# Optimization experiments

Measured on AMD Instinct MI355X. Metric: run time of the kernel, lower is better.

The kernel has to match this reference:

```python
import jax, jax.numpy as jnp
import numpy as np

EMBED = 1024
HEADS = 16
HEAD_SIZE = 64


def setup_inputs() -> dict:
    key = jax.random.key(0)
    ks = jax.random.split(key, 6)
    B, T = 2, 2048
    s = EMBED ** -0.5
    x = jax.random.normal(ks[0], (B, T, EMBED), dtype=jnp.float32)
    Wk = jax.random.normal(ks[1], (EMBED, HEADS * HEAD_SIZE), dtype=jnp.float32) * s
    Wq = jax.random.normal(ks[2], (EMBED, HEADS * HEAD_SIZE), dtype=jnp.float32) * s
    Wv = jax.random.normal(ks[3], (EMBED, HEADS * HEAD_SIZE), dtype=jnp.float32) * s
    Wp = jax.random.normal(ks[4], (HEADS * HEAD_SIZE, EMBED), dtype=jnp.float32) * s
    bp = jax.random.normal(ks[5], (EMBED,), dtype=jnp.float32) * 0.01
    return {"x": x, "Wk": Wk, "Wq": Wq, "Wv": Wv, "Wp": Wp, "bp": bp}


def reference(x, Wk, Wq, Wv, Wp, bp):
    # x: [B, T, C]; dropout in eval mode (identity), matching inference semantics
    B, T, C = x.shape
    def split_heads(y):  # [B,T,H*Dh] -> [B,H,T,Dh]
        return y.reshape(B, T, HEADS, HEAD_SIZE).transpose(0, 2, 1, 3)
    q = split_heads(x @ Wq)
    k = split_heads(x @ Wk)
    v = split_heads(x @ Wv)
    scale = HEAD_SIZE ** -0.5
    wei = jnp.einsum('bhqd,bhkd->bhqk', q, k) * scale  # [B,H,T,T]
    causal = jnp.tril(jnp.ones((T, T), dtype=bool))
    wei = jnp.where(causal, wei, -jnp.inf)
    wei = jax.nn.softmax(wei, axis=-1)
    out = jnp.einsum('bhqk,bhkd->bhqd', wei, v)  # [B,H,T,Dh]
    out = out.transpose(0, 2, 1, 3).reshape(B, T, HEADS * HEAD_SIZE)
    return out @ Wp + bp
```

## Files before the change

### kernel.cpp

```cpp
#include <hip/hip_runtime.h>
#include <stdint.h>


typedef unsigned short bfu;
typedef unsigned int u32;
typedef short bf16x8 __attribute__((ext_vector_type(8)));
typedef float f32x4 __attribute__((ext_vector_type(4)));
typedef float f32x16 __attribute__((ext_vector_type(16)));

#define DEVI static __device__ __forceinline__

DEVI bfu f2bf(float f) {
  union { float f; unsigned u; } a; a.f = f;
  unsigned u = a.u;
  u += 0x7fffu + ((u >> 16) & 1u);
  return (bfu)(u >> 16);
}

DEVI float bf2f(bfu x) {
  union { u32 u; float f; } a; a.u = ((u32)x) << 16; return a.f;
}

DEVI void gld_lds16(const void* g, void* l) {
  __builtin_amdgcn_global_load_lds(
      (const __attribute__((address_space(1))) void*)g,
      (__attribute__((address_space(3))) void*)l, 16, 0, 0);
}

#define BAR_VM4()                                         \
  do {                                                    \
    asm volatile("s_waitcnt vmcnt(4)" ::: "memory");      \
    __builtin_amdgcn_s_barrier();                         \
    asm volatile("" ::: "memory");                        \
  } while (0)
#define BAR_VM0()                                         \
  do {                                                    \
    asm volatile("s_waitcnt vmcnt(0)" ::: "memory");      \
    __builtin_amdgcn_s_barrier();                         \
    asm volatile("" ::: "memory");                        \
  } while (0)


__global__ __launch_bounds__(256) void conv_x(const float* __restrict__ x,
                                              bfu* __restrict__ xb) {
  const int n4 = (4096 * 1024) / 4;
  for (int i = blockIdx.x * 256 + threadIdx.x; i < n4; i += gridDim.x * 256) {
    float4 v = ((const float4*)x)[i];
    ushort4 p;
    p.x = f2bf(v.x); p.y = f2bf(v.y); p.z = f2bf(v.z); p.w = f2bf(v.w);
    ((ushort4*)xb)[i] = p;
  }
}

__global__ __launch_bounds__(256) void conv_w(
    const float* __restrict__ W0, const float* __restrict__ W1,
    const float* __restrict__ W2, const float* __restrict__ W3,
    bfu* __restrict__ T0, bfu* __restrict__ T1,
    bfu* __restrict__ T2, bfu* __restrict__ T3) {
  __shared__ bfu tile[64][65];
  const float* W; bfu* T;
  switch (blockIdx.z) {
    case 0:  W = W0; T = T0; break;
    case 1:  W = W1; T = T1; break;
    case 2:  W = W2; T = T2; break;
    default: W = W3; T = T3; break;
  }
  const int k0 = blockIdx.y * 64, n0 = blockIdx.x * 64;
  const int c = threadIdx.x & 63, r4 = threadIdx.x >> 6;
#pragma unroll
  for (int i = 0; i < 16; i++) {
    int row = r4 + i * 4;
    tile[row][c] = f2bf(W[(size_t)(k0 + row) * 1024 + n0 + c]);
  }
  __syncthreads();
#pragma unroll
  for (int i = 0; i < 16; i++) {
    int row = r4 + i * 4;
    T[(size_t)(n0 + row) * 1024 + k0 + c] = tile[c][row];
  }
}


__global__ __launch_bounds__(512) void gemm_qkv256(
    const bfu* __restrict__ A, const bfu* __restrict__ Bt,
    bfu* __restrict__ Qb, bfu* __restrict__ Kb, bfu* __restrict__ Vb) {
  __shared__ __align__(16) bfu LDS[2 * 32768];
  const int bid = blockIdx.x;
  const int xcd = bid & 7, i0 = bid >> 3;
  const int tx = i0 >> 1, ty = xcd * 2 + (i0 & 1);
  const int z = tx >> 2;
  const int m0 = ty * 256, n0g = tx * 256;
  const int tid = threadIdx.x, wave = tid >> 6, lane = tid & 63;
  const int wr = wave >> 2, wc = wave & 3;
  const int fr = lane & 15, fq = lane >> 4;
  const int rslot4 = fq ^ ((fr >> 1) & 3);

#define STAGE_HT(bufn, ktile, isB, kk)                                           \
  do {                                                                           \
    const bfu* srcb = (isB) ? Bt + (size_t)n0g * 1024 : A + (size_t)m0 * 1024;   \
    bfu* dstb = LDS + (bufn) * 32768 + ((isB) ? 16384 : 0) + (kk) * 8192;        \
    _Pragma("unroll")                                                            \
    for (int j_ = 0; j_ < 2; j_++) {                                             \
      int s_ = tid + j_ * 512;                                                   \
      int r_ = s_ >> 2, cg_ = (s_ & 3) ^ ((r_ >> 1) & 3);                        \
      gld_lds16(srcb + (size_t)r_ * 1024 + (ktile) * 64 + (kk) * 32 + cg_ * 8,   \
                dstb + s_ * 8);                                                  \
    }                                                                            \
  } while (0)

#define READ_B(kk)                                                               \
  _Pragma("unroll")                                                              \
  for (int n = 0; n < 4; n++)                                                    \
    bfv[n] = *(const bf16x8*)&bufc_p[16384 + (kk) * 8192 +                       \
              ((wc * 64 + n * 16 + fr) * 4 + rslot4) * 8];

#define READ_A(dst, mq, kk)                                                      \
  _Pragma("unroll")                                                              \
  for (int mm = 0; mm < 4; mm++)                                                 \
    dst[mm] = *(const bf16x8*)&bufc_p[(kk) * 8192 +                              \
              ((wr * 128 + ((mq) * 4 + mm) * 16 + fr) * 4 + rslot4) * 8];

#define MFMA_Q(afv, mq)                                                          \
  __builtin_amdgcn_s_setprio(1);                                                 \
  _Pragma("unroll")                                                              \
  for (int mm = 0; mm < 4; mm++)                                                 \
    _Pragma("unroll")                                                            \
    for (int n = 0; n < 4; n++)                                                  \
      acc[(mq) * 4 + mm][n] = __builtin_amdgcn_mfma_f32_16x16x32_bf16(           \
          afv[mm], bfv[n], acc[(mq) * 4 + mm][n], 0, 0, 0);                      \
  __builtin_amdgcn_s_setprio(0);

  f32x4 acc[8][4] = {};
  STAGE_HT(0, 0, 0, 0);
  STAGE_HT(0, 0, 1, 0);
  STAGE_HT(0, 0, 0, 1);
  STAGE_HT(0, 0, 1, 1);
  BAR_VM4();

  const int NT = 16;
  for (int t = 0; t < NT; t++) {
    const int more = (t + 1 < NT);
    const bfu* bufc_p = LDS + (t & 1) * 32768;
    const int bufn = (t & 1) ^ 1;
    bf16x8 bfv[4], afA[4], afB[4];
    READ_B(0);
    READ_A(afA, 0, 0);
    if (more) STAGE_HT(bufn, t + 1, 0, 0);
    MFMA_Q(afA, 0);
    READ_A(afB, 1, 0);
    if (more) STAGE_HT(bufn, t + 1, 1, 0);
    MFMA_Q(afB, 1);
    if (more) BAR_VM4();
    else      BAR_VM0();
    READ_B(1);
    READ_A(afA, 0, 1);
    if (more) STAGE_HT(bufn, t + 1, 0, 1);
    MFMA_Q(afA, 0);
    READ_A(afB, 1, 1);
    if (more) STAGE_HT(bufn, t + 1, 1, 1);
    MFMA_Q(afB, 1);
    BAR_VM4();
  }
#undef STAGE_HT
#undef READ_B
#undef READ_A
#undef MFMA_Q

  const float qs = (z == 0) ? 0.1803368801f : 1.0f;
#pragma unroll
  for (int mf = 0; mf < 8; mf++)
#pragma unroll
    for (int n = 0; n < 4; n++) {
      int r = m0 + wr * 128 + mf * 16 + fq * 4;
      int cwm = (tx & 3) * 256 + wc * 64 + n * 16 + fr;
      int b = r >> 11, tt = r & 2047, h = cwm >> 6, d = cwm & 63;
      if (z == 0) {
        size_t base = ((size_t)(b * 16 + h) * 2048 + tt) * 64 + d;
#pragma unroll
        for (int i = 0; i < 4; i++)
          Qb[base + (size_t)i * 64] = f2bf(acc[mf][n][i] * qs);
      } else if (z == 1) {
        size_t base = ((size_t)(b * 16 + h) * 2048 + tt) * 64 + d;
#pragma unroll
        for (int i = 0; i < 4; i++)
          Kb[base + (size_t)i * 64] = f2bf(acc[mf][n][i]);
      } else {
        size_t base = ((size_t)(b * 16 + h) * 64 + d) * 2048 + tt;
        ushort4 p;
        p.x = f2bf(acc[mf][n][0]); p.y = f2bf(acc[mf][n][1]);
        p.z = f2bf(acc[mf][n][2]); p.w = f2bf(acc[mf][n][3]);
        *(ushort4*)&Vb[base] = p;
      }
    }
}


DEVI void gemm128_core(const bfu* __restrict__ A, const bfu* __restrict__ Bt,
                       int K, int m0, int n0, bfu* As, bfu* Bs, int tid,
                       f32x4 acc[4][4]) {
  const int lane = tid & 63, wave = tid >> 6;
  const int wr = wave >> 1, wc = wave & 1;
  const int fr = lane & 15, fq = lane >> 4;
  const int r_a = tid >> 2;
  const int koff = ((tid & 3) ^ ((tid >> 3) & 3)) * 8;
  const int rslot = (fq ^ ((fr >> 1) & 3)) * 8;
#define GSTAGE(buf, k0s)                                                              \
  do {                                                                                \
    gld_lds16(A  + (size_t)(m0 +      r_a) * K + (k0s) + koff,                        \
              As + (buf) * 4096 + tid * 8);                                           \
    gld_lds16(A  + (size_t)(m0 + 64 + r_a) * K + (k0s) + koff,                        \
              As + (buf) * 4096 + 2048 + tid * 8);                                    \
    gld_lds16(Bt + (size_t)(n0 +      r_a) * K + (k0s) + koff,                        \
              Bs + (buf) * 4096 + tid * 8);                                           \
    gld_lds16(Bt + (size_t)(n0 + 64 + r_a) * K + (k0s) + koff,                        \
              Bs + (buf) * 4096 + 2048 + tid * 8);                                    \
  } while (0)
  const int NS = K >> 5;
  GSTAGE(0, 0);
  GSTAGE(1, 32);
  BAR_VM4();
  for (int i = 0; i < NS; i++) {
    if (i + 2 < NS) GSTAGE((i + 2) % 3, (i + 2) * 32);
    const bfu* AsC = As + (i % 3) * 4096;
    const bfu* BsC = Bs + (i % 3) * 4096;
    bf16x8 af[4], bfv[4];
#pragma unroll
    for (int m = 0; m < 4; m++)
      af[m] = *(const bf16x8*)&AsC[(wr * 64 + m * 16 + fr) * 32 + rslot];
#pragma unroll
    for (int n = 0; n < 4; n++)
      bfv[n] = *(const bf16x8*)&BsC[(wc * 64 + n * 16 + fr) * 32 + rslot];
#pragma unroll
    for (int m = 0; m < 4; m++)
#pragma unroll
      for (int n = 0; n < 4; n++)
        acc[m][n] = __builtin_amdgcn_mfma_f32_16x16x32_bf16(af[m], bfv[n],
                                                            acc[m][n], 0, 0, 0);
    if (i + 2 < NS) BAR_VM4();
    else            BAR_VM0();
  }
#undef GSTAGE
}

__global__ __launch_bounds__(256) void gemm_proj(
    const bfu* __restrict__ A, const bfu* __restrict__ Bt,
    const float* __restrict__ bias, float* __restrict__ out) {
  __shared__ __align__(16) bfu As[3 * 4096];
  __shared__ __align__(16) bfu Bs[3 * 4096];
  const int bid = blockIdx.x;
  const int xcd = bid & 7, i0 = bid >> 3;
  const int tx = i0 >> 2, ty = xcd * 4 + (i0 & 3);
  const int m0 = ty * 128, n0 = tx * 128;
  const int tid = threadIdx.x, lane = tid & 63, wave = tid >> 6;
  const int wr = wave >> 1, wc = wave & 1, fr = lane & 15, fq = lane >> 4;
  f32x4 acc[4][4] = {};
  gemm128_core(A, Bt, 1024, m0, n0, As, Bs, tid, acc);
#pragma unroll
  for (int m = 0; m < 4; m++)
#pragma unroll
    for (int n = 0; n < 4; n++) {
      int r = m0 + wr * 64 + m * 16 + fq * 4;
      int c = n0 + wc * 64 + n * 16 + fr;
      float bv = bias[c];
#pragma unroll
      for (int i = 0; i < 4; i++)
        out[(size_t)(r + i) * 1024 + c] = acc[m][n][i] + bv;
    }
}


__global__ __launch_bounds__(256) void attn_fwd(
    const bfu* __restrict__ Q, const bfu* __restrict__ K,
    const bfu* __restrict__ Vt, bfu* __restrict__ Ob,
    bfu* __restrict__ PO, float* __restrict__ PM, float* __restrict__ PL) {
  __shared__ __align__(16) bfu Ks[3][4096];
  __shared__ __align__(16) bfu Vs[3][4096];
  const int bid = blockIdx.x;
  const int xcd = bid & 7, i0 = bid >> 3;
  const int slot = i0 >> 5, cuL = i0 & 31;
  const int head = cuL >> 3, cu8 = cuL & 7;
  const int hb = xcd * 4 + head;
  int qb, mode;
  if (slot < 2)      { qb = 15 - cu8; mode = slot + 1; }
  else if (cu8 < 4)  { if (slot == 3) return; qb = cu8; mode = 0; }
  else               { qb = cu8; mode = slot - 1; }
  const int kb0   = (mode == 2) ? (qb + 1) : 0;
  const int kbmax = (mode == 1) ? qb : (2 * qb + 1);
  const int tid = threadIdx.x, wave = tid >> 6, lane = tid & 63;
  const int q31 = lane & 31, hi = lane >> 5;
  const bfu* Qh = Q  + (size_t)hb * 2048 * 64;
  const bfu* Kh = K  + (size_t)hb * 2048 * 64;
  const bfu* Vh = Vt + (size_t)hb * 64 * 2048;
  const int b = hb >> 4, h = hb & 15;
  const int q0w = qb * 128 + wave * 32;
  const int qg = q0w + q31;

  const int r0 = tid >> 3, r1 = (256 + tid) >> 3;
  const int c0 = (tid & 7) ^ (r0 & 7), c1 = (tid & 7) ^ (r1 & 7);
#define STAGE_K(bufi, kbase)                                                          \
  do {                                                                                \
    gld_lds16(Kh + (size_t)((kbase) + r0) * 64 + c0 * 8, &Ks[bufi][tid * 8]);         \
    gld_lds16(Kh + (size_t)((kbase) + r1) * 64 + c1 * 8, &Ks[bufi][(256 + tid) * 8]); \
  } while (0)
#define STAGE_V(bufi, kbase)                                                          \
  do {                                                                                \
    gld_lds16(Vh + (size_t)r0 * 2048 + (kbase) + c0 * 8, &Vs[bufi][tid * 8]);         \
    gld_lds16(Vh + (size_t)r1 * 2048 + (kbase) + c1 * 8, &Vs[bufi][(256 + tid) * 8]); \
  } while (0)

  bf16x8 qv[4];
#pragma unroll
  for (int c = 0; c < 4; c++)
    qv[c] = *(const bf16x8*)&Qh[(size_t)(q0w + q31) * 64 + c * 16 + hi * 8];

  bf16x8 onesv;
#pragma unroll
  for (int j = 0; j < 8; j++) onesv[j] = (short)0x3F80;

  f32x16 o0 = {}, o1 = {}, lac = {};
  float m = -1e30f;

  STAGE_K(0, kb0 * 64);
  STAGE_V(0, kb0 * 64);
  STAGE_K(1, (kb0 + 1) * 64);
  STAGE_V(1, (kb0 + 1) * 64);
  BAR_VM4();

  for (int kb = kb0; kb <= kbmax; kb++) {
    const int idx = kb - kb0;
    const int cur = idx % 3, nxt = (idx + 2) % 3;
    const int pre = (kb + 2 <= kbmax);
    const int kbase = kb * 64;
    const int active = (kbase <= q0w + 31);
    const bfu* KsC = Ks[cur];
    const bfu* VsC = Vs[cur];
    if (pre) STAGE_K(nxt, (kb + 2) * 64);
    u32 W0[8], W1[8];
    if (active) {
      f32x16 s0 = {}, s1 = {};
#pragma unroll
      for (int c = 0; c < 4; c++) {
        const int g = 2 * c + hi;
        bf16x8 kf0 = *(const bf16x8*)&KsC[(q31 * 8 + (g ^ (q31 & 7))) * 8];
        bf16x8 kf1 = *(const bf16x8*)&KsC[((32 + q31) * 8 + (g ^ (q31 & 7))) * 8];
        s0 = __builtin_amdgcn_mfma_f32_32x32x16_bf16(kf0, qv[c], s0, 0, 0, 0);
        s1 = __builtin_amdgcn_mfma_f32_32x32x16_bf16(kf1, qv[c], s1, 0, 0, 0);
      }
      if (kbase + 63 > q0w) {
#pragma unroll
        for (int r = 0; r < 16; r++) {
          int krow = (r & 3) + 8 * (r >> 2) + 4 * hi;
          if (kbase + krow > qg)      s0[r] = -1e30f;
          if (kbase + 32 + krow > qg) s1[r] = -1e30f;
        }
      }
      float pm = s0[0];
#pragma unroll
      for (int r = 1; r < 16; r++) pm = fmaxf(pm, s0[r]);
#pragma unroll
      for (int r = 0; r < 16; r++) pm = fmaxf(pm, s1[r]);
      pm = fmaxf(pm, __shfl_xor(pm, 32));
      if (!__all(pm <= m + 8.0f)) {
        float mn = fmaxf(m, pm);
        float al = __builtin_amdgcn_exp2f(m - mn);
        m = mn;
#pragma unroll
        for (int r = 0; r < 16; r++) {
          float alq = __shfl(al, (r & 3) + 8 * (r >> 2) + 4 * hi);
          o0[r] *= alq; o1[r] *= alq; lac[r] *= alq;
        }
      }
#pragma unroll
      for (int w = 0; w < 8; w++) {
        float a0 = __builtin_amdgcn_exp2f(s0[2 * w] - m);
        float a1 = __builtin_amdgcn_exp2f(s0[2 * w + 1] - m);
        asm("v_cvt_pk_bf16_f32 %0, %1, %2" : "=v"(W0[w]) : "v"(a0), "v"(a1));
        float b0 = __builtin_amdgcn_exp2f(s1[2 * w] - m);
        float b1 = __builtin_amdgcn_exp2f(s1[2 * w + 1] - m);
        asm("v_cvt_pk_bf16_f32 %0, %1, %2" : "=v"(W1[w]) : "v"(b0), "v"(b1));
      }
    }
    if (pre) STAGE_V(nxt, (kb + 2) * 64);
    if (active) {
      __builtin_amdgcn_s_setprio(1);
#pragma unroll
      for (int c = 0; c < 4; c++) {
        const u32* Wsel = (c < 2) ? W0 : W1;
        const int w0 = 4 * (c & 1);
        u32 t0 = Wsel[w0],     t2 = Wsel[w0 + 2];
        u32 t1 = Wsel[w0 + 1], t3 = Wsel[w0 + 3];
        asm("v_permlane32_swap_b32 %0, %1" : "+v"(t0), "+v"(t2));
        asm("v_permlane32_swap_b32 %0, %1" : "+v"(t1), "+v"(t3));
        union { u32 u[4]; bf16x8 v; } pa;
        pa.u[0] = t0; pa.u[1] = t1; pa.u[2] = t2; pa.u[3] = t3;
        const int g = 2 * c + hi;
        bf16x8 vb0 = *(const bf16x8*)&VsC[(q31 * 8 + (g ^ (q31 & 7))) * 8];
        bf16x8 vb1 = *(const bf16x8*)&VsC[((32 + q31) * 8 + (g ^ (q31 & 7))) * 8];
        o0  = __builtin_amdgcn_mfma_f32_32x32x16_bf16(pa.v, vb0,   o0,  0, 0, 0);
        o1  = __builtin_amdgcn_mfma_f32_32x32x16_bf16(pa.v, vb1,   o1,  0, 0, 0);
        lac = __builtin_amdgcn_mfma_f32_32x32x16_bf16(pa.v, onesv, lac, 0, 0, 0);
      }
      __builtin_amdgcn_s_setprio(0);
    }
    if (pre) BAR_VM4();
    else     BAR_VM0();
  }
#undef STAGE_K
#undef STAGE_V

  if (mode == 0) {
#pragma unroll
    for (int r = 0; r < 16; r++) {
      int t = q0w + (r & 3) + 8 * (r >> 2) + 4 * hi;
      float inv = 1.0f / lac[r];
      size_t base = (size_t)(b * 2048 + t) * 1024 + h * 64;
      Ob[base + q31]      = f2bf(o0[r] * inv);
      Ob[base + 32 + q31] = f2bf(o1[r] * inv);
    }
  } else {
    const int p = (hb * 12 + (qb - 4)) * 2 + (mode - 1);
    bfu*   po = PO + (size_t)p * 8192;
    float* pmv = PM + p * 128;
    float* plv = PL + p * 128;
    pmv[wave * 32 + q31] = m;
#pragma unroll
    for (int r = 0; r < 16; r++) {
      int rm = (r & 3) + 8 * (r >> 2) + 4 * hi;
      plv[wave * 32 + rm] = lac[r];
      po[(wave * 32 + rm) * 64 + q31]      = f2bf(o0[r]);
      po[(wave * 32 + rm) * 64 + 32 + q31] = f2bf(o1[r]);
    }
  }
}

__global__ __launch_bounds__(256) void attn_comb(
    const bfu* __restrict__ PO, const float* __restrict__ PM,
    const float* __restrict__ PL, bfu* __restrict__ Ob) {
  const int g = blockIdx.x;
  const int hb = g / 12, j = g % 12, qb = j + 4;
  const int b = hb >> 4, h = hb & 15;
  const int p0 = g * 2, p1 = p0 + 1;
  const int tid = threadIdx.x;
  const int r = tid >> 1, ch = tid & 1;
  float m0 = PM[p0 * 128 + r], m1 = PM[p1 * 128 + r];
  float l0 = PL[p0 * 128 + r], l1 = PL[p1 * 128 + r];
  float ms = fmaxf(m0, m1);
  float f0 = __builtin_amdgcn_exp2f(m0 - ms);
  float f1 = __builtin_amdgcn_exp2f(m1 - ms);
  float inv = 1.0f / (l0 * f0 + l1 * f1);
  const bfu* a0 = PO + (size_t)p0 * 8192 + r * 64 + ch * 32;
  const bfu* a1 = PO + (size_t)p1 * 8192 + r * 64 + ch * 32;
  const int t = qb * 128 + r;
  bfu* ob = Ob + (size_t)(b * 2048 + t) * 1024 + h * 64 + ch * 32;
#pragma unroll
  for (int k = 0; k < 4; k++) {
    bf16x8 v0 = *(const bf16x8*)(a0 + k * 8);
    bf16x8 v1 = *(const bf16x8*)(a1 + k * 8);
    bf16x8 vo;
#pragma unroll
    for (int e = 0; e < 8; e++) {
      float acc = bf2f((bfu)(unsigned short)v0[e]) * f0 +
                  bf2f((bfu)(unsigned short)v1[e]) * f1;
      vo[e] = (short)f2bf(acc * inv);
    }
    *(bf16x8*)(ob + k * 8) = vo;
  }
}


extern "C" void kernel_launch(void* const* d_in, const int* in_sizes, int n_in,
                              void* d_out, int out_size, void* d_ws, size_t ws_size,
                              hipStream_t stream) {
  const float* x  = (const float*)d_in[0];
  const float* Wk = (const float*)d_in[1];
  const float* Wq = (const float*)d_in[2];
  const float* Wv = (const float*)d_in[3];
  const float* Wp = (const float*)d_in[4];
  const float* bp = (const float*)d_in[5];
  char* ws = (char*)d_ws;
  bfu* xb  = (bfu*)(ws);
  bfu* Wqt = (bfu*)(ws + ( 8u << 20));
  bfu* Wkt = (bfu*)(ws + (10u << 20));
  bfu* Wvt = (bfu*)(ws + (12u << 20));
  bfu* Wpt = (bfu*)(ws + (14u << 20));
  bfu* Qb  = (bfu*)(ws + (16u << 20));
  bfu* Kb  = (bfu*)(ws + (24u << 20));
  bfu* Vb  = (bfu*)(ws + (32u << 20));
  bfu* Ab  = (bfu*)(ws + (40u << 20));
  bfu*   PO = (bfu*)(ws);
  float* PM = (float*)(ws + (13u << 20));
  float* PL = (float*)(ws + (13u << 20) + (512u << 10));
  float* out = (float*)d_out;

  conv_x<<<1024, 256, 0, stream>>>(x, xb);
  conv_w<<<dim3(16, 16, 4), 256, 0, stream>>>(Wq, Wk, Wv, Wp, Wqt, Wkt, Wvt, Wpt);
  gemm_qkv256<<<192, 512, 0, stream>>>(xb, Wqt, Qb, Kb, Vb);
  attn_fwd<<<1024, 256, 0, stream>>>(Qb, Kb, Vb, Ab, PO, PM, PL);
  attn_comb<<<384, 256, 0, stream>>>(PO, PM, PL, Ab);
  gemm_proj<<<256, 256, 0, stream>>>(Ab, Wpt, bp, out);
}
```

Baseline: 121.1 us.

## Rewrite projection GEMM with 512 threads, double-buffered K=64 tiles and split staging

The output projection GEMM goes from 256 to 512 threads per block, each of the 8 waves computing a 32x64 sub-tile. K advances in 64-wide tiles held in two LDS buffers. Each tile's loads are split into half-stages that are interleaved with MFMA groups, which run under raised s_setprio. The goal is more waves to hide latency and better overlap of loads with compute, at the cost of more barriers per K tile and fewer accumulators per wave.

```diff
diff --git a/kernel.cpp b/kernel.cpp
--- a/kernel.cpp
+++ b/kernel.cpp
@@ -30,6 +30,12 @@
 #define BAR_VM4()                                         \
   do {                                                    \
     asm volatile("s_waitcnt vmcnt(4)" ::: "memory");      \
+    __builtin_amdgcn_s_barrier();                         \
+    asm volatile("" ::: "memory");                        \
+  } while (0)
+#define BAR_VM2()                                         \
+  do {                                                    \
+    asm volatile("s_waitcnt vmcnt(2)" ::: "memory");      \
     __builtin_amdgcn_s_barrier();                         \
     asm volatile("" ::: "memory");                        \
   } while (0)
@@ -195,76 +201,94 @@
 }
 
 
-DEVI void gemm128_core(const bfu* __restrict__ A, const bfu* __restrict__ Bt,
-                       int K, int m0, int n0, bfu* As, bfu* Bs, int tid,
-                       f32x4 acc[4][4]) {
-  const int lane = tid & 63, wave = tid >> 6;
-  const int wr = wave >> 1, wc = wave & 1;
-  const int fr = lane & 15, fq = lane >> 4;
-  const int r_a = tid >> 2;
-  const int koff = ((tid & 3) ^ ((tid >> 3) & 3)) * 8;
-  const int rslot = (fq ^ ((fr >> 1) & 3)) * 8;
-#define GSTAGE(buf, k0s)                                                              \
-  do {                                                                                \
-    gld_lds16(A  + (size_t)(m0 +      r_a) * K + (k0s) + koff,                        \
-              As + (buf) * 4096 + tid * 8);                                           \
-    gld_lds16(A  + (size_t)(m0 + 64 + r_a) * K + (k0s) + koff,                        \
-              As + (buf) * 4096 + 2048 + tid * 8);                                    \
-    gld_lds16(Bt + (size_t)(n0 +      r_a) * K + (k0s) + koff,                        \
-              Bs + (buf) * 4096 + tid * 8);                                           \
-    gld_lds16(Bt + (size_t)(n0 + 64 + r_a) * K + (k0s) + koff,                        \
-              Bs + (buf) * 4096 + 2048 + tid * 8);                                    \
-  } while (0)
-  const int NS = K >> 5;
-  GSTAGE(0, 0);
-  GSTAGE(1, 32);
-  BAR_VM4();
-  for (int i = 0; i < NS; i++) {
-    if (i + 2 < NS) GSTAGE((i + 2) % 3, (i + 2) * 32);
-    const bfu* AsC = As + (i % 3) * 4096;
-    const bfu* BsC = Bs + (i % 3) * 4096;
-    bf16x8 af[4], bfv[4];
-#pragma unroll
-    for (int m = 0; m < 4; m++)
-      af[m] = *(const bf16x8*)&AsC[(wr * 64 + m * 16 + fr) * 32 + rslot];
-#pragma unroll
-    for (int n = 0; n < 4; n++)
-      bfv[n] = *(const bf16x8*)&BsC[(wc * 64 + n * 16 + fr) * 32 + rslot];
-#pragma unroll
-    for (int m = 0; m < 4; m++)
-#pragma unroll
-      for (int n = 0; n < 4; n++)
-        acc[m][n] = __builtin_amdgcn_mfma_f32_16x16x32_bf16(af[m], bfv[n],
-                                                            acc[m][n], 0, 0, 0);
-    if (i + 2 < NS) BAR_VM4();
-    else            BAR_VM0();
-  }
-#undef GSTAGE
-}
-
-__global__ __launch_bounds__(256) void gemm_proj(
+__global__ __launch_bounds__(512) void gemm_proj(
     const bfu* __restrict__ A, const bfu* __restrict__ Bt,
     const float* __restrict__ bias, float* __restrict__ out) {
-  __shared__ __align__(16) bfu As[3 * 4096];
-  __shared__ __align__(16) bfu Bs[3 * 4096];
+  __shared__ __align__(16) bfu LDS[2 * 16384];
   const int bid = blockIdx.x;
   const int xcd = bid & 7, i0 = bid >> 3;
   const int tx = i0 >> 2, ty = xcd * 4 + (i0 & 3);
   const int m0 = ty * 128, n0 = tx * 128;
-  const int tid = threadIdx.x, lane = tid & 63, wave = tid >> 6;
-  const int wr = wave >> 1, wc = wave & 1, fr = lane & 15, fq = lane >> 4;
-  f32x4 acc[4][4] = {};
-  gemm128_core(A, Bt, 1024, m0, n0, As, Bs, tid, acc);
-#pragma unroll
-  for (int m = 0; m < 4; m++)
+  const int tid = threadIdx.x, wave = tid >> 6, lane = tid & 63;
+  const int wr = wave >> 1, wc = wave & 1;
+  const int fr = lane & 15, fq = lane >> 4;
+  const int rslot4 = fq ^ ((fr >> 1) & 3);
+
+#define STAGE_HT(bufn, ktile, isB, kk)                                           \
+  do {                                                                           \
+    const bfu* srcb = (isB) ? Bt + (size_t)n0 * 1024 : A + (size_t)m0 * 1024;    \
+    bfu* dstb = LDS + (bufn) * 16384 + ((isB) ? 8192 : 0) + (kk) * 4096;         \
+    int r_ = tid >> 2, cg_ = (tid & 3) ^ ((r_ >> 1) & 3);                        \
+    gld_lds16(srcb + (size_t)r_ * 1024 + (ktile) * 64 + (kk) * 32 + cg_ * 8,     \
+              dstb + tid * 8);                                                   \
+  } while (0)
+
+#define READ_B(kk)                                                               \
+  _Pragma("unroll")                                                              \
+  for (int n = 0; n < 4; n++)                                                    \
+    bfv[n] = *(const bf16x8*)&bufc_p[8192 + (kk) * 4096 +                        \
+              ((wc * 64 + n * 16 + fr) * 4 + rslot4) * 8];
+
+#define READ_A(kk)                                                               \
+  _Pragma("unroll")                                                              \
+  for (int mm = 0; mm < 2; mm++)                                                 \
+    af[mm] = *(const bf16x8*)&bufc_p[(kk) * 4096 +                               \
+              ((wr * 32 + mm * 16 + fr) * 4 + rslot4) * 8];
+
+#define MFMA_H(nq)                                                               \
+  __builtin_amdgcn_s_setprio(1);                                                 \
+  _Pragma("unroll")                                                              \
+  for (int mm = 0; mm < 2; mm++)                                                 \
+    _Pragma("unroll")                                                            \
+    for (int n = 0; n < 2; n++)                                                  \
+      acc[mm][(nq) * 2 + n] = __builtin_amdgcn_mfma_f32_16x16x32_bf16(           \
+          af[mm], bfv[(nq) * 2 + n], acc[mm][(nq) * 2 + n], 0, 0, 0);            \
+  __builtin_amdgcn_s_setprio(0);
+
+  f32x4 acc[2][4] = {};
+  STAGE_HT(0, 0, 0, 0);
+  STAGE_HT(0, 0, 1, 0);
+  STAGE_HT(0, 0, 0, 1);
+  STAGE_HT(0, 0, 1, 1);
+  BAR_VM2();
+
+  const int NT = 16;
+  for (int t = 0; t < NT; t++) {
+    const int more = (t + 1 < NT);
+    const bfu* bufc_p = LDS + (t & 1) * 16384;
+    const int bufn = (t & 1) ^ 1;
+    bf16x8 bfv[4], af[2];
+    READ_B(0);
+    READ_A(0);
+    if (more) STAGE_HT(bufn, t + 1, 0, 0);
+    MFMA_H(0);
+    if (more) STAGE_HT(bufn, t + 1, 1, 0);
+    MFMA_H(1);
+    if (more) BAR_VM2();
+    else      BAR_VM0();
+    READ_B(1);
+    READ_A(1);
+    if (more) STAGE_HT(bufn, t + 1, 0, 1);
+    MFMA_H(0);
+    if (more) STAGE_HT(bufn, t + 1, 1, 1);
+    MFMA_H(1);
+    BAR_VM2();
+  }
+#undef STAGE_HT
+#undef READ_B
+#undef READ_A
+#undef MFMA_H
+
+#pragma unroll
+  for (int mm = 0; mm < 2; mm++)
 #pragma unroll
     for (int n = 0; n < 4; n++) {
-      int r = m0 + wr * 64 + m * 16 + fq * 4;
+      int r = m0 + wr * 32 + mm * 16 + fq * 4;
       int c = n0 + wc * 64 + n * 16 + fr;
       float bv = bias[c];
 #pragma unroll
       for (int i = 0; i < 4; i++)
-        out[(size_t)(r + i) * 1024 + c] = acc[m][n][i] + bv;
+        out[(size_t)(r + i) * 1024 + c] = acc[mm][n][i] + bv;
     }
 }
 
@@ -497,5 +521,5 @@
   gemm_qkv256<<<192, 512, 0, stream>>>(xb, Wqt, Qb, Kb, Vb);
   attn_fwd<<<1024, 256, 0, stream>>>(Qb, Kb, Vb, Ab, PO, PM, PL);
   attn_comb<<<384, 256, 0, stream>>>(PO, PM, PL, Ab);
-  gemm_proj<<<256, 256, 0, stream>>>(Ab, Wpt, bp, out);
-}
+  gemm_proj<<<256, 512, 0, stream>>>(Ab, Wpt, bp, out);
+}
```

Measured after the change: 113.4 us. -6.3%, faster.
